# Optimization experiments

Hardware: AMD Instinct MI355X
Metric: run time of the kernel (lower is better)

## Reference

```python
import jax, jax.numpy as jnp
import numpy as np

B, DIM_Z, N_SAMPLES = 256, 64, 32
LOG_2PI = float(np.log(2.0 * np.pi))
VAR_EPS = 0.0001


def log_pdf(mean, logvar, zs):
    # elementwise Gaussian log-density (per dim), matching torch log_pdf
    return -0.5 * LOG_2PI - 0.5 * logvar - (zs - mean) ** 2 / (2.0 * jnp.exp(logvar) + VAR_EPS)


def setup_inputs() -> dict:
    key = jax.random.key(0)
    k1, k2, k3, k4, k5 = jax.random.split(key, 5)
    return {
        "prior_mean": jax.random.normal(k1, (B, DIM_Z), dtype=jnp.float32),
        "prior_logvar": jax.random.normal(k2, (B, DIM_Z), dtype=jnp.float32),
        "post_mean": jax.random.normal(k3, (B, DIM_Z), dtype=jnp.float32),
        "post_logvar": jax.random.normal(k4, (B, DIM_Z), dtype=jnp.float32),
        "eps": jax.random.normal(k5, (B, DIM_Z, N_SAMPLES), dtype=jnp.float32),
    }


def reference(prior_mean, prior_logvar, post_mean, post_logvar, eps):
    batch_size = post_mean.shape[0]
    # reparameterized samples from each posterior: [B, D, S]
    zs = post_mean[:, :, None] + eps * jnp.exp(0.5 * post_logvar)[:, :, None]
    # log p_prior_j(z_{j,d,s}): [B, D, S]
    logp_priors_zs = log_pdf(prior_mean[:, :, None], prior_logvar[:, :, None], zs)
    # log p_post_i(z_{j,d,s}): [B(i), B(j), D, S] -- the big broadcast intermediate
    logp_posts_zs = log_pdf(post_mean[:, None, :, None], post_logvar[:, None, :, None], zs[None])
    # max-stabilized log-mean-exp over posteriors i == logsumexp - log(B)
    logp_agg_post_zs = jax.scipy.special.logsumexp(logp_posts_zs, axis=0) - jnp.log(
        jnp.asarray(batch_size, dtype=logp_posts_zs.dtype)
    )  # [B(j), D, S]
    density_gaps = logp_agg_post_zs - logp_priors_zs  # [B, D, S]
    kl = density_gaps.mean(axis=0)  # [D, S]
    kl = kl.sum(axis=0).mean(axis=-1)  # scalar
    return kl
```

## Files before the change

kernel.cpp:

```cpp
#include <hip/hip_runtime.h>
#include <math.h>

#define BATCH 256
#define DIMZ  64
#define NSAMP 32
#define JB    8

__global__ __launch_bounds__(256) void lpo_kl_kernel(
    const float* __restrict__ prior_mean,
    const float* __restrict__ prior_logvar,
    const float* __restrict__ post_mean,
    const float* __restrict__ post_logvar,
    const float* __restrict__ eps,
    float* __restrict__ out)
{
    constexpr float LOG_2PI = 1.8378770664093453f;
    constexpr float VAR_EPS = 1e-4f;
    constexpr float LOG2E   = 1.4426950408889634f;
    constexpr float LN2     = 0.6931471805599453f;
    constexpr float LOG_B   = 5.545177444479562f;

    __shared__ __align__(16) float m_s[BATCH];
    __shared__ __align__(16) float a_s[BATCH];
    __shared__ __align__(16) float v_s[BATCH];
    __shared__ float sg_s[BATCH];
    __shared__ float wred[4];

    const int tid = threadIdx.x;
    const int d   = blockIdx.x & (DIMZ - 1);
    const int j0  = (blockIdx.x >> 6) * JB;

    {
        const int i = tid;
        float m   = post_mean[i * DIMZ + d];
        float lv  = post_logvar[i * DIMZ + d];
        float den = 2.0f * __expf(lv) + VAR_EPS;
        float c1n = -0.5f * LOG_2PI - 0.5f * lv;
        m_s[i]  = m;
        a_s[i]  = c1n * den;
        v_s[i]  = LOG2E / den;
        sg_s[i] = __expf(0.5f * lv);
    }
    __syncthreads();

    const int s  = tid & (NSAMP - 1);
    const int jj = tid >> 5;
    const int j  = j0 + jj;

    const float z = m_s[j] + eps[(j * DIMZ + d) * NSAMP + s] * sg_s[j];

    float sum0 = 0.f, sum1 = 0.f, sum2 = 0.f, sum3 = 0.f;
    #pragma unroll 4
    for (int i = 0; i < BATCH; i += 4) {
        const float4 mv = *(const float4*)(m_s + i);
        const float4 av = *(const float4*)(a_s + i);
        const float4 iv = *(const float4*)(v_s + i);
        float d0 = z - mv.x; sum0 += __builtin_amdgcn_exp2f((av.x - d0 * d0) * iv.x);
        float d1 = z - mv.y; sum1 += __builtin_amdgcn_exp2f((av.y - d1 * d1) * iv.y);
        float d2 = z - mv.z; sum2 += __builtin_amdgcn_exp2f((av.z - d2 * d2) * iv.z);
        float d3 = z - mv.w; sum3 += __builtin_amdgcn_exp2f((av.w - d3 * d3) * iv.w);
    }
    const float sum = (sum0 + sum1) + (sum2 + sum3);

    const float pm   = prior_mean[j * DIMZ + d];
    const float plv  = prior_logvar[j * DIMZ + d];
    const float pden = 2.0f * __expf(plv) + VAR_EPS;
    const float dz   = z - pm;
    const float logp_prior = -0.5f * LOG_2PI - 0.5f * plv - dz * dz / pden;

    const float lse_nat = LN2 * __builtin_amdgcn_logf(sum) - LOG_B;
    float contrib = (lse_nat - logp_prior) * (1.0f / (BATCH * NSAMP));

    for (int off = 32; off > 0; off >>= 1)
        contrib += __shfl_down(contrib, off);
    if ((tid & 63) == 0) wred[tid >> 6] = contrib;
    __syncthreads();
    if (tid == 0)
        atomicAdd(out, (wred[0] + wred[1]) + (wred[2] + wred[3]));
}

extern "C" void kernel_launch(void* const* d_in, const int* in_sizes, int n_in,
                              void* d_out, int out_size, void* d_ws, size_t ws_size,
                              hipStream_t stream) {
    const float* prior_mean   = (const float*)d_in[0];
    const float* prior_logvar = (const float*)d_in[1];
    const float* post_mean    = (const float*)d_in[2];
    const float* post_logvar  = (const float*)d_in[3];
    const float* eps          = (const float*)d_in[4];
    float* out = (float*)d_out;

    hipMemsetAsync(out, 0, sizeof(float), stream);

    lpo_kl_kernel<<<dim3((BATCH / JB) * DIMZ), dim3(256), 0, stream>>>(
        prior_mean, prior_logvar, post_mean, post_logvar, eps, out);
}
```

Measured before the change: 95.12 us.

## Expand quadratic exponent into FMA form and process four samples per thread

```diff
diff --git a/kernel.cpp b/kernel.cpp
--- a/kernel.cpp
+++ b/kernel.cpp
@@ -4,7 +4,7 @@
 #define BATCH 256
 #define DIMZ  64
 #define NSAMP 32
-#define JB    8
+#define JB    32
 
 __global__ __launch_bounds__(256) void lpo_kl_kernel(
     const float* __restrict__ prior_mean,
@@ -20,9 +20,10 @@
     constexpr float LN2     = 0.6931471805599453f;
     constexpr float LOG_B   = 5.545177444479562f;
 
-    __shared__ __align__(16) float m_s[BATCH];
-    __shared__ __align__(16) float a_s[BATCH];
-    __shared__ __align__(16) float v_s[BATCH];
+    __shared__ __align__(16) float A_s[BATCH];
+    __shared__ __align__(16) float B_s[BATCH];
+    __shared__ __align__(16) float C_s[BATCH];
+    __shared__ float m_s[BATCH];
     __shared__ float sg_s[BATCH];
     __shared__ float wred[4];
 
@@ -31,45 +32,67 @@
     const int j0  = (blockIdx.x >> 6) * JB;
 
     {
-        const int i = tid;
+        const int i   = tid;
         float m   = post_mean[i * DIMZ + d];
         float lv  = post_logvar[i * DIMZ + d];
         float den = 2.0f * __expf(lv) + VAR_EPS;
-        float c1n = -0.5f * LOG_2PI - 0.5f * lv;
+        float C   = LOG2E / den;
+        float B   = 2.0f * m * C;
+        float A   = LOG2E * (-0.5f * LOG_2PI - 0.5f * lv) - m * m * C;
+        A_s[i]  = A;
+        B_s[i]  = B;
+        C_s[i]  = C;
         m_s[i]  = m;
-        a_s[i]  = c1n * den;
-        v_s[i]  = LOG2E / den;
         sg_s[i] = __expf(0.5f * lv);
     }
     __syncthreads();
 
     const int s  = tid & (NSAMP - 1);
     const int jj = tid >> 5;
-    const int j  = j0 + jj;
 
-    const float z = m_s[j] + eps[(j * DIMZ + d) * NSAMP + s] * sg_s[j];
+    float z[4], nz2[4];
+    #pragma unroll
+    for (int k = 0; k < 4; ++k) {
+        const int j = j0 + jj + 8 * k;
+        z[k]   = m_s[j] + eps[(j * DIMZ + d) * NSAMP + s] * sg_s[j];
+        nz2[k] = -(z[k] * z[k]);
+    }
 
-    float sum0 = 0.f, sum1 = 0.f, sum2 = 0.f, sum3 = 0.f;
-    #pragma unroll 4
+    float acc[4][4] = {};
+    #pragma unroll 2
     for (int i = 0; i < BATCH; i += 4) {
-        const float4 mv = *(const float4*)(m_s + i);
-        const float4 av = *(const float4*)(a_s + i);
-        const float4 iv = *(const float4*)(v_s + i);
-        float d0 = z - mv.x; sum0 += __builtin_amdgcn_exp2f((av.x - d0 * d0) * iv.x);
-        float d1 = z - mv.y; sum1 += __builtin_amdgcn_exp2f((av.y - d1 * d1) * iv.y);
-        float d2 = z - mv.z; sum2 += __builtin_amdgcn_exp2f((av.z - d2 * d2) * iv.z);
-        float d3 = z - mv.w; sum3 += __builtin_amdgcn_exp2f((av.w - d3 * d3) * iv.w);
+        const float4 Av = *(const float4*)(A_s + i);
+        const float4 Bv = *(const float4*)(B_s + i);
+        const float4 Cv = *(const float4*)(C_s + i);
+        #pragma unroll
+        for (int k = 0; k < 4; ++k) {
+            acc[0][k] += __builtin_amdgcn_exp2f(
+                __builtin_fmaf(Cv.x, nz2[k], __builtin_fmaf(Bv.x, z[k], Av.x)));
+            acc[1][k] += __builtin_amdgcn_exp2f(
+                __builtin_fmaf(Cv.y, nz2[k], __builtin_fmaf(Bv.y, z[k], Av.y)));
+            acc[2][k] += __builtin_amdgcn_exp2f(
+                __builtin_fmaf(Cv.z, nz2[k], __builtin_fmaf(Bv.z, z[k], Av.z)));
+            acc[3][k] += __builtin_amdgcn_exp2f(
+                __builtin_fmaf(Cv.w, nz2[k], __builtin_fmaf(Bv.w, z[k], Av.w)));
+        }
     }
-    const float sum = (sum0 + sum1) + (sum2 + sum3);
 
-    const float pm   = prior_mean[j * DIMZ + d];
-    const float plv  = prior_logvar[j * DIMZ + d];
-    const float pden = 2.0f * __expf(plv) + VAR_EPS;
-    const float dz   = z - pm;
-    const float logp_prior = -0.5f * LOG_2PI - 0.5f * plv - dz * dz / pden;
+    float contrib = 0.0f;
+    #pragma unroll
+    for (int k = 0; k < 4; ++k) {
+        const int j = j0 + jj + 8 * k;
+        const float sum = (acc[0][k] + acc[1][k]) + (acc[2][k] + acc[3][k]);
+        const float lse_nat = LN2 * __builtin_amdgcn_logf(sum) - LOG_B;
 
-    const float lse_nat = LN2 * __builtin_amdgcn_logf(sum) - LOG_B;
-    float contrib = (lse_nat - logp_prior) * (1.0f / (BATCH * NSAMP));
+        const float pm   = prior_mean[j * DIMZ + d];
+        const float plv  = prior_logvar[j * DIMZ + d];
+        const float pden = 2.0f * __expf(plv) + VAR_EPS;
+        const float dz   = z[k] - pm;
+        const float logp_prior = -0.5f * LOG_2PI - 0.5f * plv - dz * dz / pden;
+
+        contrib += lse_nat - logp_prior;
+    }
+    contrib *= 1.0f / (BATCH * NSAMP);
 
     for (int off = 32; off > 0; off >>= 1)
         contrib += __shfl_down(contrib, off);
```

Result: faster. 86.54 us (-9.0%).
